# Optimization experiments

Hardware: AMD Instinct MI355X
Metric: run time of the kernel (lower is better)

The kernel has to match this reference:

```python
import jax, jax.numpy as jnp
import numpy as np

HIDDEN = 2048
INTER = 1408
NUM_EXPERTS = 8
TOP_K = 2


def setup_inputs() -> dict:
    key = jax.random.key(0)
    k_x, k_rw, k_gu, k_dn = jax.random.split(key, 4)
    x = jax.random.normal(k_x, (2, 2048, HIDDEN), dtype=jnp.float32)
    router_weight = jax.random.normal(k_rw, (NUM_EXPERTS, HIDDEN), dtype=jnp.float32)
    gate_up_proj = jax.random.normal(k_gu, (NUM_EXPERTS, 2 * INTER, HIDDEN), dtype=jnp.float32) * 0.02
    down_proj = jax.random.normal(k_dn, (NUM_EXPERTS, HIDDEN, INTER), dtype=jnp.float32) * 0.02
    return {"x": x, "router_weight": router_weight, "gate_up_proj": gate_up_proj, "down_proj": down_proj}


def reference(x, router_weight, gate_up_proj, down_proj):
    E = router_weight.shape[0]
    xf = x.reshape(-1, x.shape[-1])  # [T, D]
    # Router: logits -> float32 softmax -> top-k -> renormalize
    logits = jnp.einsum('td,ed->te', xf, router_weight)
    scores = jax.nn.softmax(logits.astype(jnp.float32), axis=-1)
    topv, topi = jax.lax.top_k(scores, TOP_K)          # [T, K]
    topv = topv / jnp.sum(topv, axis=-1, keepdims=True)
    topv = topv.astype(logits.dtype)
    # Combine weights per (token, expert): zero for unselected experts,
    # so dense per-expert compute below reproduces the sparse dispatch math.
    comb = jnp.einsum('tk,tke->te', topv, jax.nn.one_hot(topi, E, dtype=topv.dtype))  # [T, E]
    # Per-expert SwiGLU FFN, dense over experts
    gu = jnp.einsum('td,efd->etf', xf, gate_up_proj)    # [E, T, 2*inter]
    gate, up = jnp.split(gu, 2, axis=-1)
    h = jax.nn.silu(gate) * up                          # [E, T, inter]
    eo = jnp.einsum('eti,edi->etd', h, down_proj)       # [E, T, D]
    out = jnp.einsum('etd,te->td', eo, comb)            # [T, D]
    return out
```

## Files before the change

### kernel.cpp

```cpp
#include <hip/hip_runtime.h>
#include <hip/hip_bf16.h>
#include <stdint.h>

#define HIDDEN 2048
#define INTER  1408
#define NE     8
#define NTOK   4096
#define MAXT   40

typedef __attribute__((ext_vector_type(8))) short short8;
typedef __attribute__((ext_vector_type(4))) float f32x4;

typedef const __attribute__((address_space(1))) unsigned char* gp1_t;
typedef __attribute__((address_space(3))) unsigned char* lp3_t;

__device__ __forceinline__ void lds_cp16(const void* g, void* l) {
    __builtin_amdgcn_global_load_lds((gp1_t)g, (lp3_t)l, 16, 0, 0);
}

__device__ __forceinline__ float bf2f(short s) {
    union { float f; unsigned u; } u; u.u = ((unsigned)(unsigned short)s) << 16; return u.f;
}

#define C1 (NE * 2 * INTER * HIDDEN / 4)
#define C2 (NE * HIDDEN * INTER / 4)
__global__ void cvt_w_kernel(const float* __restrict__ gu, const float* __restrict__ dn,
                             __hip_bfloat16* __restrict__ gub, __hip_bfloat16* __restrict__ dnb) {
    long c = (long)blockIdx.x * blockDim.x + threadIdx.x;
    const float* s; __hip_bfloat16* d; long o;
    if (c < C1) { s = gu; d = gub; o = c; }
    else        { s = dn; d = dnb; o = c - C1; }
    o *= 4;
    float4 v = *(const float4*)(s + o);
    *(__hip_bfloat162*)(d + o)     = __float22bfloat162_rn(make_float2(v.x, v.y));
    *(__hip_bfloat162*)(d + o + 2) = __float22bfloat162_rn(make_float2(v.z, v.w));
}

__global__ void router_kernel(const float* __restrict__ x, const float* __restrict__ rw,
                              int* __restrict__ counts, int* __restrict__ topk_e,
                              float* __restrict__ topk_w, __hip_bfloat16* __restrict__ xb) {
    int wave = threadIdx.x >> 6;
    int lane = threadIdx.x & 63;
    int t = blockIdx.x * 4 + wave;
    const float4* xr = (const float4*)(x + (size_t)t * HIDDEN);
    __hip_bfloat16* xbr = xb + (size_t)t * HIDDEN;
    float acc[NE] = {0.f,0.f,0.f,0.f,0.f,0.f,0.f,0.f};
    #pragma unroll
    for (int c = lane; c < HIDDEN / 4; c += 64) {
        float4 v = xr[c];
        *(__hip_bfloat162*)(xbr + c * 4)     = __float22bfloat162_rn(make_float2(v.x, v.y));
        *(__hip_bfloat162*)(xbr + c * 4 + 2) = __float22bfloat162_rn(make_float2(v.z, v.w));
        #pragma unroll
        for (int e = 0; e < NE; ++e) {
            float4 w = ((const float4*)(rw + e * HIDDEN))[c];
            acc[e] += v.x * w.x + v.y * w.y + v.z * w.z + v.w * w.w;
        }
    }
    #pragma unroll
    for (int e = 0; e < NE; ++e) {
        #pragma unroll
        for (int off = 32; off > 0; off >>= 1) acc[e] += __shfl_xor(acc[e], off, 64);
    }
    if (lane == 0) {
        int i1 = 0; float v1 = acc[0];
        for (int e = 1; e < NE; ++e) if (acc[e] > v1) { v1 = acc[e]; i1 = e; }
        int i2 = -1; float v2 = -3.0e38f;
        for (int e = 0; e < NE; ++e) if (e != i1 && acc[e] > v2) { v2 = acc[e]; i2 = e; }
        float w1 = 1.f / (1.f + expf(v2 - v1));
        float w2 = 1.f - w1;
        topk_e[t * 2 + 0] = i1; topk_e[t * 2 + 1] = i2;
        topk_w[t * 2 + 0] = w1; topk_w[t * 2 + 1] = w2;
        atomicAdd(&counts[i1], 1);
        atomicAdd(&counts[i2], 1);
    }
}

__global__ void scan_kernel(const int* __restrict__ counts, int* __restrict__ offsets,
                            int* __restrict__ cursor, int* __restrict__ tiles,
                            int* __restrict__ n_tiles) {
    if (threadIdx.x == 0) {
        int s = 0, nt = 0;
        for (int e = 0; e < NE; ++e) {
            offsets[e] = s; cursor[e] = s;
            int c = counts[e]; s += c;
            for (int mt = 0; mt * 256 < c; ++mt) tiles[nt++] = (e << 16) | mt;
        }
        n_tiles[0] = nt;
    }
}

__global__ void scatter_kernel(const int* __restrict__ topk_e, const float* __restrict__ topk_w,
                               int* __restrict__ cursor, int* __restrict__ slot_tid,
                               float* __restrict__ slot_w, int* __restrict__ tok2slot) {
    int k = blockIdx.x * blockDim.x + threadIdx.x;
    if (k >= NTOK * 2) return;
    int e = topk_e[k];
    int slot = atomicAdd(&cursor[e], 1);
    slot_tid[slot] = k >> 1;
    slot_w[slot]   = topk_w[k];
    tok2slot[k]    = slot;
}


#define FENCE asm volatile("" ::: "memory")
#define W_V8  asm volatile("s_waitcnt vmcnt(8)" ::: "memory")
#define W_V4  asm volatile("s_waitcnt vmcnt(4)" ::: "memory")
#define W_V0  asm volatile("s_waitcnt vmcnt(0)" ::: "memory")
#define W_NONE do {} while (0)
#define BAR do { __builtin_amdgcn_sched_barrier(0); FENCE; \
                 __builtin_amdgcn_s_barrier(); FENCE; } while (0)
#define LGKM0 do { asm volatile("s_waitcnt lgkmcnt(0)" ::: "memory"); \
                   __builtin_amdgcn_sched_barrier(0); } while (0)

#define DSA(Rg, mf) (*(const short8*)((Rg) + laneA + (mf) * 512))
#define DSB(Rg, nf) (*(const short8*)((Rg) + laneB + (nf) * 512))

#define MFMA16(NFP) do { \
    __builtin_amdgcn_s_setprio(1); \
    _Pragma("unroll") \
    for (int mf_ = 0; mf_ < 8; ++mf_) { \
        acc[mf_][(NFP)*2+0] = __builtin_amdgcn_mfma_f32_16x16x32_bf16(afr[mf_], bfr[0], acc[mf_][(NFP)*2+0], 0, 0, 0); \
        acc[mf_][(NFP)*2+1] = __builtin_amdgcn_mfma_f32_16x16x32_bf16(afr[mf_], bfr[1], acc[mf_][(NFP)*2+1], 0, 0, 0); \
    } \
    __builtin_amdgcn_s_setprio(0); \
    __builtin_amdgcn_sched_barrier(0); \
} while (0)

#define KTILE(T, S01, S23, W1, W3) do { \
    const int b_ = (T) & 1; \
    const __hip_bfloat16* RA0_ = smem + (((b_ << 2) | 0) << 13); \
    const __hip_bfloat16* RA1_ = smem + (((b_ << 2) | 1) << 13); \
    const __hip_bfloat16* RB0_ = smem + (((b_ << 2) | 2) << 13); \
    const __hip_bfloat16* RB1_ = smem + (((b_ << 2) | 3) << 13); \
     \
    _Pragma("unroll") for (int mf_ = 0; mf_ < 8; ++mf_) afr[mf_] = DSA(RA0_, mf_); \
    bfr[0] = DSB(RB0_, 0); bfr[1] = DSB(RB0_, 1); \
    if (S01) stage(0, 1, (T) + 1, b_ ^ 1); \
    LGKM0; MFMA16(0); BAR; \
     \
    bfr[0] = DSB(RB0_, 2); bfr[1] = DSB(RB0_, 3); \
    if (S01) stage(1, 1, (T) + 1, b_ ^ 1); \
    LGKM0; MFMA16(1); \
    W1; BAR; \
     \
    _Pragma("unroll") for (int mf_ = 0; mf_ < 8; ++mf_) afr[mf_] = DSA(RA1_, mf_); \
    bfr[0] = DSB(RB1_, 0); bfr[1] = DSB(RB1_, 1); \
    if (S23) stage(0, 0, (T) + 2, b_); \
    LGKM0; MFMA16(0); BAR; \
     \
    bfr[0] = DSB(RB1_, 2); bfr[1] = DSB(RB1_, 3); \
    if (S23) stage(1, 0, (T) + 2, b_); \
    LGKM0; MFMA16(1); \
    W3; BAR; \
} while (0)

template<int WHICH>
__global__ __launch_bounds__(512, 2) void moe_gemm(
    const __hip_bfloat16* __restrict__ Ag,
    const __hip_bfloat16* __restrict__ Bg,
    const int* __restrict__ counts, const int* __restrict__ offsets,
    const int* __restrict__ tiles, const int* __restrict__ n_tiles,
    const int* __restrict__ slot_tid, const float* __restrict__ slot_w,
    __hip_bfloat16* __restrict__ Out)
{
    constexpr int KDIM = (WHICH == 1) ? HIDDEN : INTER;
    constexpr int NT   = KDIM / 64;

    const int ti = blockIdx.y;
    if (ti >= n_tiles[0]) return;
    const int tile = tiles[ti];
    const int e  = tile >> 16;
    const int mt = tile & 0xffff;
    const int nt = blockIdx.x;
    const int count = counts[e];
    const int off = offsets[e];

    extern __shared__ __hip_bfloat16 smem[];

    const int tid  = threadIdx.x;
    const int wave = tid >> 6;
    const int lane = tid & 63;
    const int wm = wave >> 2, wn = wave & 3;
    const int l15 = lane & 15;
    const int q   = lane >> 4;
    const int sw  = (l15 >> 1) & 3;

    const int laneA = (wm * 128 + l15) * 32 + ((q ^ sw) << 3);
    const int laneB = (wn * 64  + l15) * 32 + ((q ^ sw) << 3);

    const __hip_bfloat16* PA[2];
    const __hip_bfloat16* PB[2];
    #pragma unroll
    for (int j = 0; j < 2; ++j) {
        int cs  = j * 512 + tid;
        int row = cs >> 2;
        int kc  = (cs & 3) ^ ((row >> 1) & 3);
        int rg  = mt * 256 + row;
        int rc  = rg < count ? rg : count - 1;
        if constexpr (WHICH == 1) {
            int tok = slot_tid[off + rc];
            PA[j] = Ag + (size_t)tok * HIDDEN + kc * 8;
            int p = row >> 5, sel = (row >> 4) & 1, idx = row & 15;
            int hc = nt * 128 + p * 16 + idx;
            int grow = sel ? (INTER + hc) : hc;
            PB[j] = Bg + ((size_t)(e * 2 * INTER + grow)) * HIDDEN + kc * 8;
        } else {
            PA[j] = Ag + (size_t)(off + rc) * INTER + kc * 8;
            PB[j] = Bg + ((size_t)(e * HIDDEN + nt * 256 + row)) * INTER + kc * 8;
        }
    }

    auto stage = [&](int m, int kh, int kt, int b) {
        __hip_bfloat16* L = smem + (size_t)(((b << 2) | (m << 1) | kh) << 13);
        const __hip_bfloat16* s0 = (m ? PB[0] : PA[0]) + kt * 64 + kh * 32;
        const __hip_bfloat16* s1 = (m ? PB[1] : PA[1]) + kt * 64 + kh * 32;
        lds_cp16(s0, L + tid * 8);
        lds_cp16(s1, L + (512 + tid) * 8);
    };

    f32x4 acc[8][4];
    #pragma unroll
    for (int mf = 0; mf < 8; ++mf)
        #pragma unroll
        for (int nf = 0; nf < 4; ++nf) acc[mf][nf] = (f32x4)0.f;

    short8 afr[8], bfr[2];

    stage(0, 0, 0, 0); stage(1, 0, 0, 0);
    stage(0, 1, 0, 0); stage(1, 1, 0, 0);
    stage(0, 0, 1, 1); stage(1, 0, 1, 1);
    W_V8; BAR;

    #pragma unroll 2
    for (int t = 0; t < NT - 2; ++t) {
        KTILE(t, 1, 1, W_V8, W_V8);
    }
    KTILE(NT - 2, 1, 0, W_V8, W_V4);
    KTILE(NT - 1, 0, 0, W_V0, W_NONE);
    W_V0;

    if constexpr (WHICH == 1) {
        #pragma unroll
        for (int mf = 0; mf < 8; ++mf) {
            #pragma unroll
            for (int reg = 0; reg < 4; ++reg) {
                int row = wm * 128 + mf * 16 + q * 4 + reg;
                int rg  = mt * 256 + row;
                if (rg < count) {
                    float wgt = slot_w[off + rg];
                    #pragma unroll
                    for (int g = 0; g < 2; ++g) {
                        float gv = acc[mf][2 * g + 0][reg];
                        float uv = acc[mf][2 * g + 1][reg];
                        float hv = gv / (1.f + __expf(-gv)) * uv * wgt;
                        Out[(size_t)(off + rg) * INTER + nt * 128 + (wn * 2 + g) * 16 + l15] =
                            __float2bfloat16(hv);
                    }
                }
            }
        }
    } else {
        #pragma unroll
        for (int mf = 0; mf < 8; ++mf) {
            #pragma unroll
            for (int reg = 0; reg < 4; ++reg) {
                int row = wm * 128 + mf * 16 + q * 4 + reg;
                int rg  = mt * 256 + row;
                if (rg < count) {
                    size_t base = (size_t)(off + rg) * HIDDEN + nt * 256 + wn * 64;
                    #pragma unroll
                    for (int nf = 0; nf < 4; ++nf)
                        Out[base + nf * 16 + l15] = __float2bfloat16(acc[mf][nf][reg]);
                }
            }
        }
    }
}

__global__ void combine_kernel(const __hip_bfloat16* __restrict__ eo,
                               const int* __restrict__ tok2slot,
                               float* __restrict__ out) {
    int idx = blockIdx.x * blockDim.x + threadIdx.x;
    int t = idx >> 8;
    int c = (idx & 255) * 8;
    int s1 = tok2slot[t * 2], s2 = tok2slot[t * 2 + 1];
    short8 v1 = *(const short8*)(eo + (size_t)s1 * HIDDEN + c);
    short8 v2 = *(const short8*)(eo + (size_t)s2 * HIDDEN + c);
    float4 o0, o1;
    o0.x = bf2f(v1[0]) + bf2f(v2[0]); o0.y = bf2f(v1[1]) + bf2f(v2[1]);
    o0.z = bf2f(v1[2]) + bf2f(v2[2]); o0.w = bf2f(v1[3]) + bf2f(v2[3]);
    o1.x = bf2f(v1[4]) + bf2f(v2[4]); o1.y = bf2f(v1[5]) + bf2f(v2[5]);
    o1.z = bf2f(v1[6]) + bf2f(v2[6]); o1.w = bf2f(v1[7]) + bf2f(v2[7]);
    float* op = out + (size_t)t * HIDDEN + c;
    *(float4*)op = o0;
    *(float4*)(op + 4) = o1;
}

extern "C" void kernel_launch(void* const* d_in, const int* in_sizes, int n_in,
                              void* d_out, int out_size, void* d_ws, size_t ws_size,
                              hipStream_t stream)
{
    (void)in_sizes; (void)n_in; (void)ws_size; (void)out_size;
    const float* x  = (const float*)d_in[0];
    const float* rw = (const float*)d_in[1];
    const float* gu = (const float*)d_in[2];
    const float* dn = (const float*)d_in[3];

    char* p = (char*)d_ws;
    auto take = [&](size_t bytes) { char* r = p; p += (bytes + 255) & ~(size_t)255; return r; };
    __hip_bfloat16* xb  = (__hip_bfloat16*)take((size_t)NTOK * HIDDEN * 2);
    __hip_bfloat16* gub = (__hip_bfloat16*)take((size_t)NE * 2 * INTER * HIDDEN * 2);
    __hip_bfloat16* dnb = (__hip_bfloat16*)take((size_t)NE * HIDDEN * INTER * 2);
    __hip_bfloat16* hbuf= (__hip_bfloat16*)take((size_t)(2 * NTOK + 256) * INTER * 2);
    int*   counts   = (int*)take(64);
    int*   offsets  = (int*)take(64);
    int*   cursor   = (int*)take(64);
    int*   ntile    = (int*)take(64);
    int*   tiles    = (int*)take(MAXT * 4);
    int*   topk_e   = (int*)take((size_t)NTOK * 2 * 4);
    float* topk_w   = (float*)take((size_t)NTOK * 2 * 4);
    int*   slot_tid = (int*)take((size_t)(2 * NTOK + 256) * 4);
    float* slot_w   = (float*)take((size_t)(2 * NTOK + 256) * 4);
    int*   tok2slot = (int*)take((size_t)NTOK * 2 * 4);
    __hip_bfloat16* eo = gub;

    hipFuncSetAttribute((const void*)moe_gemm<1>,
                        hipFuncAttributeMaxDynamicSharedMemorySize, 131072);
    hipFuncSetAttribute((const void*)moe_gemm<2>,
                        hipFuncAttributeMaxDynamicSharedMemorySize, 131072);

    hipMemsetAsync(counts, 0, 64, stream);

    cvt_w_kernel<<<dim3((C1 + C2) / 256), 256, 0, stream>>>(gu, dn, gub, dnb);

    router_kernel<<<dim3(NTOK / 4), 256, 0, stream>>>(x, rw, counts, topk_e, topk_w, xb);
    scan_kernel<<<dim3(1), 64, 0, stream>>>(counts, offsets, cursor, tiles, ntile);
    scatter_kernel<<<dim3((NTOK * 2) / 256), 256, 0, stream>>>(topk_e, topk_w, cursor,
                                                               slot_tid, slot_w, tok2slot);

    moe_gemm<1><<<dim3(INTER / 128, MAXT), 512, 131072, stream>>>(
        xb, gub, counts, offsets, tiles, ntile, slot_tid, slot_w, hbuf);
    moe_gemm<2><<<dim3(HIDDEN / 256, MAXT), 512, 131072, stream>>>(
        hbuf, dnb, counts, offsets, tiles, ntile, slot_tid, slot_w, eo);
    combine_kernel<<<dim3(NTOK * HIDDEN / 8 / 256), 256, 0, stream>>>(
        eo, tok2slot, (float*)d_out);
}
```

Measured before the change: 667.8 us.

## Restructure MoE GEMM K-loop into two half-tile phases with single barrier each

```diff
diff --git a/kernel.cpp b/kernel.cpp
--- a/kernel.cpp
+++ b/kernel.cpp
@@ -103,55 +103,31 @@
 
 
 #define FENCE asm volatile("" ::: "memory")
-#define W_V8  asm volatile("s_waitcnt vmcnt(8)" ::: "memory")
 #define W_V4  asm volatile("s_waitcnt vmcnt(4)" ::: "memory")
 #define W_V0  asm volatile("s_waitcnt vmcnt(0)" ::: "memory")
-#define W_NONE do {} while (0)
 #define BAR do { __builtin_amdgcn_sched_barrier(0); FENCE; \
-                 __builtin_amdgcn_s_barrier(); FENCE; } while (0)
-#define LGKM0 do { asm volatile("s_waitcnt lgkmcnt(0)" ::: "memory"); \
-                   __builtin_amdgcn_sched_barrier(0); } while (0)
+                 __builtin_amdgcn_s_barrier(); FENCE; \
+                 __builtin_amdgcn_sched_barrier(0); } while (0)
 
 #define DSA(Rg, mf) (*(const short8*)((Rg) + laneA + (mf) * 512))
 #define DSB(Rg, nf) (*(const short8*)((Rg) + laneB + (nf) * 512))
 
-#define MFMA16(NFP) do { \
-    __builtin_amdgcn_s_setprio(1); \
-    _Pragma("unroll") \
-    for (int mf_ = 0; mf_ < 8; ++mf_) { \
-        acc[mf_][(NFP)*2+0] = __builtin_amdgcn_mfma_f32_16x16x32_bf16(afr[mf_], bfr[0], acc[mf_][(NFP)*2+0], 0, 0, 0); \
-        acc[mf_][(NFP)*2+1] = __builtin_amdgcn_mfma_f32_16x16x32_bf16(afr[mf_], bfr[1], acc[mf_][(NFP)*2+1], 0, 0, 0); \
-    } \
-    __builtin_amdgcn_s_setprio(0); \
-    __builtin_amdgcn_sched_barrier(0); \
-} while (0)
-
-#define KTILE(T, S01, S23, W1, W3) do { \
-    const int b_ = (T) & 1; \
-    const __hip_bfloat16* RA0_ = smem + (((b_ << 2) | 0) << 13); \
-    const __hip_bfloat16* RA1_ = smem + (((b_ << 2) | 1) << 13); \
-    const __hip_bfloat16* RB0_ = smem + (((b_ << 2) | 2) << 13); \
-    const __hip_bfloat16* RB1_ = smem + (((b_ << 2) | 3) << 13); \
-     \
-    _Pragma("unroll") for (int mf_ = 0; mf_ < 8; ++mf_) afr[mf_] = DSA(RA0_, mf_); \
-    bfr[0] = DSB(RB0_, 0); bfr[1] = DSB(RB0_, 1); \
-    if (S01) stage(0, 1, (T) + 1, b_ ^ 1); \
-    LGKM0; MFMA16(0); BAR; \
-     \
-    bfr[0] = DSB(RB0_, 2); bfr[1] = DSB(RB0_, 3); \
-    if (S01) stage(1, 1, (T) + 1, b_ ^ 1); \
-    LGKM0; MFMA16(1); \
-    W1; BAR; \
-     \
-    _Pragma("unroll") for (int mf_ = 0; mf_ < 8; ++mf_) afr[mf_] = DSA(RA1_, mf_); \
-    bfr[0] = DSB(RB1_, 0); bfr[1] = DSB(RB1_, 1); \
-    if (S23) stage(0, 0, (T) + 2, b_); \
-    LGKM0; MFMA16(0); BAR; \
-     \
-    bfr[0] = DSB(RB1_, 2); bfr[1] = DSB(RB1_, 3); \
-    if (S23) stage(1, 0, (T) + 2, b_); \
-    LGKM0; MFMA16(1); \
-    W3; BAR; \
+#define PHASE(T, KH, DOSTAGE, DOWAIT, DOBAR) do {                            \
+    const int b_ = (T) & 1;                                                  \
+    const __hip_bfloat16* RA_ = smem + (((b_ << 2) | (KH)) << 13);           \
+    const __hip_bfloat16* RB_ = smem + (((b_ << 2) | 2 | (KH)) << 13);       \
+    short8 afr[8], bfr[4];                                                   \
+    _Pragma("unroll") for (int mf_ = 0; mf_ < 8; ++mf_) afr[mf_] = DSA(RA_, mf_); \
+    _Pragma("unroll") for (int nf_ = 0; nf_ < 4; ++nf_) bfr[nf_] = DSB(RB_, nf_); \
+    if (DOSTAGE) { stage(0, (KH), (T) + 1, b_ ^ 1); stage(1, (KH), (T) + 1, b_ ^ 1); } \
+    __builtin_amdgcn_s_setprio(1);                                           \
+    _Pragma("unroll") for (int mf_ = 0; mf_ < 8; ++mf_)                      \
+        _Pragma("unroll") for (int nf_ = 0; nf_ < 4; ++nf_)                  \
+            acc[mf_][nf_] = __builtin_amdgcn_mfma_f32_16x16x32_bf16(         \
+                afr[mf_], bfr[nf_], acc[mf_][nf_], 0, 0, 0);                 \
+    __builtin_amdgcn_s_setprio(0);                                           \
+    if ((DOWAIT) == 4) { W_V4; } else if ((DOWAIT) < 0) { W_V0; }            \
+    if (DOBAR) { BAR; }                                                      \
 } while (0)
 
 template<int WHICH>
@@ -224,20 +200,17 @@
         #pragma unroll
         for (int nf = 0; nf < 4; ++nf) acc[mf][nf] = (f32x4)0.f;
 
-    short8 afr[8], bfr[2];
-
     stage(0, 0, 0, 0); stage(1, 0, 0, 0);
     stage(0, 1, 0, 0); stage(1, 1, 0, 0);
-    stage(0, 0, 1, 1); stage(1, 0, 1, 1);
-    W_V8; BAR;
+    W_V4; BAR;
 
     #pragma unroll 2
-    for (int t = 0; t < NT - 2; ++t) {
-        KTILE(t, 1, 1, W_V8, W_V8);
-    }
-    KTILE(NT - 2, 1, 0, W_V8, W_V4);
-    KTILE(NT - 1, 0, 0, W_V0, W_NONE);
-    W_V0;
+    for (int t = 0; t < NT - 1; ++t) {
+        PHASE(t, 0, 1, 4, 1);
+        PHASE(t, 1, 1, 4, 1);
+    }
+    PHASE(NT - 1, 0, 0, -1, 1);
+    PHASE(NT - 1, 1, 0, 0, 0);
 
     if constexpr (WHICH == 1) {
         #pragma unroll
```

Measured after the change: 674.4 us. No clear change (+1.0%).
